# Kernel optimization log

Hardware: AMD Instinct MI355X
Metric: run time of the kernel (lower is better)

Reference implementation:

```python
import jax, jax.numpy as jnp
import numpy as np

D = 512; H = 8; DFF = 2048; S1 = 1024; S2 = 512; B = 8; EPS = 1e-5


def setup_inputs() -> dict:
    key = jax.random.key(0)
    ks = jax.random.split(key, 10)
    def w(k, shape):
        return jax.random.normal(k, shape, dtype=jnp.float32) * 0.02
    return {
        "rna_embed": jax.random.normal(ks[0], (S1, B, D), dtype=jnp.float32),
        "protein_embed": jax.random.normal(ks[1], (S2, B, D), dtype=jnp.float32),
        # self-attention params (torch MHA packed in_proj)
        "Wqkv_s": w(ks[2], (3 * D, D)), "bqkv_s": jnp.zeros((3 * D,), jnp.float32),
        "Wo_s": w(ks[3], (D, D)), "bo_s": jnp.zeros((D,), jnp.float32),
        # cross-attention params
        "Wqkv_c": w(ks[4], (3 * D, D)), "bqkv_c": jnp.zeros((3 * D,), jnp.float32),
        "Wo_c": w(ks[5], (D, D)), "bo_c": jnp.zeros((D,), jnp.float32),
        # FFN params
        "W1": w(ks[6], (DFF, D)), "b1": jnp.zeros((DFF,), jnp.float32),
        "W2": w(ks[7], (D, DFF)), "b2": jnp.zeros((D,), jnp.float32),
        # LayerNorm params: norm0_1, norm1_1, norm1_2, norm2
        "g0": jnp.ones((D,), jnp.float32), "be0": jnp.zeros((D,), jnp.float32),
        "g11": jnp.ones((D,), jnp.float32), "be11": jnp.zeros((D,), jnp.float32),
        "g12": jnp.ones((D,), jnp.float32), "be12": jnp.zeros((D,), jnp.float32),
        "g2": jnp.ones((D,), jnp.float32), "be2": jnp.zeros((D,), jnp.float32),
    }


def _layernorm(x, g, b):
    m = jnp.mean(x, axis=-1, keepdims=True)
    v = jnp.mean(jnp.square(x - m), axis=-1, keepdims=True)
    return (x - m) * jax.lax.rsqrt(v + EPS) * g + b


def _mha(xq, xkv, Wqkv, bqkv, Wo, bo):
    # xq: (Sq, B, D), xkv: (Sk, B, D)
    Wq, Wk, Wv = jnp.split(Wqkv, 3, axis=0)
    bq, bk, bv = jnp.split(bqkv, 3)
    hd = D // H
    scale = 1.0 / np.sqrt(hd).astype(np.float32)
    q = (xq @ Wq.T + bq).reshape(xq.shape[0], -1, H, hd)   # (Sq,B,H,hd)
    k = (xkv @ Wk.T + bk).reshape(xkv.shape[0], -1, H, hd)  # (Sk,B,H,hd)
    v = (xkv @ Wv.T + bv).reshape(xkv.shape[0], -1, H, hd)
    scores = jnp.einsum('qbhd,kbhd->bhqk', q, k) * scale    # (B,H,Sq,Sk)
    attn = jax.nn.softmax(scores, axis=-1)
    o = jnp.einsum('bhqk,kbhd->qbhd', attn, v).reshape(xq.shape[0], -1, D)
    return o @ Wo.T + bo


def reference(rna_embed, protein_embed, Wqkv_s, bqkv_s, Wo_s, bo_s,
              Wqkv_c, bqkv_c, Wo_c, bo_c, W1, b1, W2, b2,
              g0, be0, g11, be11, g12, be12, g2, be2):
    x1 = rna_embed
    # pre-norm self-attention
    h = _layernorm(x1, g0, be0)
    x1 = x1 + _mha(h, h, Wqkv_s, bqkv_s, Wo_s, bo_s)
    # pre-norm cross-attention (queries from x1, keys/values from protein)
    x1 = x1 + _mha(_layernorm(x1, g11, be11), _layernorm(protein_embed, g12, be12),
                   Wqkv_c, bqkv_c, Wo_c, bo_c)
    # pre-norm FFN
    h = _layernorm(x1, g2, be2)
    x1 = x1 + (jax.nn.relu(h @ W1.T + b1) @ W2.T + b2)
    return x1
```

## Files before the change

kernel.cpp:

```cpp
#include <hip/hip_runtime.h>

typedef unsigned short u16;
typedef unsigned int u32;
typedef u16 u16x8 __attribute__((ext_vector_type(8)));
typedef u16 u16x4 __attribute__((ext_vector_type(4)));
typedef short bfx8 __attribute__((ext_vector_type(8)));
typedef float f32x4 __attribute__((ext_vector_type(4)));

#define AS1 __attribute__((address_space(1)))
#define AS3 __attribute__((address_space(3)))

__device__ __forceinline__ u16 f2bf(float f) {
  union { float f; u32 u; } c; c.f = f;
  u32 u = c.u;
  u += 0x7fffu + ((u >> 16) & 1u);
  return (u16)(u >> 16);
}

__device__ __forceinline__ float bf2f(u16 b) {
  union { u32 u; float f; } c; c.u = ((u32)b) << 16;
  return c.f;
}

__device__ __forceinline__ u32 cvt_pk_bf16(float lo, float hi) {
  u32 r;
  asm("v_cvt_pk_bf16_f32 %0, %1, %2" : "=v"(r) : "v"(lo), "v"(hi));
  return r;
}

__device__ __forceinline__ float fexp2(float x) {
  float r;
  asm("v_exp_f32 %0, %1" : "=v"(r) : "v"(x));
  return r;
}

__device__ __forceinline__ void ln_core(float f[8], const float* __restrict__ g,
                                        const float* __restrict__ be,
                                        u16* __restrict__ out, int gw, int lane) {
  float s = 0.f, q = 0.f;
#pragma unroll
  for (int e = 0; e < 8; ++e) { s += f[e]; q += f[e] * f[e]; }
#pragma unroll
  for (int m = 1; m < 64; m <<= 1) { s += __shfl_xor(s, m); q += __shfl_xor(q, m); }
  float mean = s * (1.f / 512.f);
  float var = q * (1.f / 512.f) - mean * mean;
  float rs = rsqrtf(var + 1e-5f);
  const float4* g4 = (const float4*)g;
  const float4* b4 = (const float4*)be;
  float4 ga = g4[2 * lane], gb = g4[2 * lane + 1];
  float4 ba = b4[2 * lane], bb = b4[2 * lane + 1];
  float gv[8] = {ga.x, ga.y, ga.z, ga.w, gb.x, gb.y, gb.z, gb.w};
  float bv[8] = {ba.x, ba.y, ba.z, ba.w, bb.x, bb.y, bb.z, bb.w};
  u16x8 o;
#pragma unroll
  for (int e = 0; e < 8; ++e) o[e] = f2bf((f[e] - mean) * rs * gv[e] + bv[e]);
  ((u16x8*)(out + (size_t)gw * 512))[lane] = o;
}

__device__ __forceinline__ void ln_row_f32(const float* __restrict__ x, const float* __restrict__ g,
                                           const float* __restrict__ be, u16* __restrict__ out,
                                           int gw, int lane) {
  const float4* row = (const float4*)(x + (size_t)gw * 512);
  float4 a = row[2 * lane], b = row[2 * lane + 1];
  float f[8] = {a.x, a.y, a.z, a.w, b.x, b.y, b.z, b.w};
  ln_core(f, g, be, out, gw, lane);
}

__device__ __forceinline__ void ln_row_bf16(const u16* __restrict__ x, const float* __restrict__ g,
                                            const float* __restrict__ be, u16* __restrict__ out,
                                            int gw, int lane) {
  u16x8 v = ((const u16x8*)(x + (size_t)gw * 512))[lane];
  float f[8];
#pragma unroll
  for (int e = 0; e < 8; ++e) f[e] = bf2f(v[e]);
  ln_core(f, g, be, out, gw, lane);
}

__global__ __launch_bounds__(256) void cvtln_kernel(const float* __restrict__ a0, const float* __restrict__ a1,
                                                    const float* __restrict__ a2, const float* __restrict__ a3,
                                                    const float* __restrict__ a4, const float* __restrict__ a5,
                                                    u16* __restrict__ b0, u16* __restrict__ b1,
                                                    u16* __restrict__ b2, u16* __restrict__ b3,
                                                    u16* __restrict__ b4, u16* __restrict__ b5,
                                                    const float* __restrict__ x, const float* __restrict__ g,
                                                    const float* __restrict__ be, u16* __restrict__ lnout) {
  if (blockIdx.x < 4096) {
    int i = blockIdx.x * 256 + threadIdx.x;
    const float* s; u16* d; int off;
    if      (i < 196608) { s = a0; d = b0; off = i; }
    else if (i < 262144) { s = a1; d = b1; off = i - 196608; }
    else if (i < 458752) { s = a2; d = b2; off = i - 262144; }
    else if (i < 524288) { s = a3; d = b3; off = i - 458752; }
    else if (i < 786432) { s = a4; d = b4; off = i - 524288; }
    else                 { s = a5; d = b5; off = i - 786432; }
    float4 v = ((const float4*)s)[off];
    u16x4 o;
    o[0] = f2bf(v.x); o[1] = f2bf(v.y); o[2] = f2bf(v.z); o[3] = f2bf(v.w);
    ((u16x4*)d)[off] = o;
  } else {
    int gw = ((blockIdx.x - 4096) * 256 + threadIdx.x) >> 6;
    ln_row_f32(x, g, be, lnout, gw, threadIdx.x & 63);
  }
}

__global__ __launch_bounds__(256) void lnb_kernel(const u16* __restrict__ x,
                                                  const float* __restrict__ g,
                                                  const float* __restrict__ be,
                                                  u16* __restrict__ out, int ntok) {
  int gw = (blockIdx.x * 256 + threadIdx.x) >> 6;
  if (gw >= ntok) return;
  ln_row_bf16(x, g, be, out, gw, threadIdx.x & 63);
}

__global__ __launch_bounds__(256) void ln2_kernel(const u16* __restrict__ xa, const float* __restrict__ ga,
                                                  const float* __restrict__ ba, u16* __restrict__ oa,
                                                  const float* __restrict__ xb, const float* __restrict__ gb,
                                                  const float* __restrict__ bb, u16* __restrict__ ob) {
  int lane = threadIdx.x & 63;
  if (blockIdx.x < 2048) {
    int gw = (blockIdx.x * 256 + threadIdx.x) >> 6;
    ln_row_bf16(xa, ga, ba, oa, gw, lane);
  } else {
    int gw = ((blockIdx.x - 2048) * 256 + threadIdx.x) >> 6;
    ln_row_f32(xb, gb, bb, ob, gw, lane);
  }
}

__global__ __launch_bounds__(256) void vt_kernel(const u16* __restrict__ vB, u16* __restrict__ vt,
                                                 int stride, int S) {
  __shared__ u16 lt[64 * 68];
  const int t = threadIdx.x;
  const int b = blockIdx.y, h = blockIdx.z;
  const int sr = t >> 3, dc = (t & 7) * 8;
#pragma unroll
  for (int p = 0; p < 2; ++p) {
    int s = blockIdx.x * 64 + sr + p * 32;
    u16x8 v = *(const u16x8*)(vB + (size_t)(s * 8 + b) * stride + h * 64 + dc);
    u16x4 lo, hi;
    lo[0]=v[0]; lo[1]=v[1]; lo[2]=v[2]; lo[3]=v[3];
    hi[0]=v[4]; hi[1]=v[5]; hi[2]=v[6]; hi[3]=v[7];
    *(u16x4*)&lt[(sr + p * 32) * 68 + dc] = lo;
    *(u16x4*)&lt[(sr + p * 32) * 68 + dc + 4] = hi;
  }
  __syncthreads();
#pragma unroll
  for (int p = 0; p < 2; ++p) {
    int d = sr + p * 32;
    u16x8 o;
#pragma unroll
    for (int e = 0; e < 8; ++e) o[e] = lt[(dc + e) * 68 + d];
    *(u16x8*)(vt + ((size_t)(b * 8 + h) * 64 + d) * S + blockIdx.x * 64 + dc) = o;
  }
}

template <int EPI, int BM, int BN>
__device__ __forceinline__ void gemm8_body(const u16* __restrict__ A,
                                           const u16* __restrict__ Bw,
                                           const float* __restrict__ bias,
                                           const void* __restrict__ res,
                                           void* __restrict__ Cout,
                                           int M, int K, int bn, int bm) {
  constexpr int WCg = BN / 64;
  constexpr int WRg = 8 / WCg;
  constexpr int RPW = BM / WRg;
  constexpr int IM = RPW / 16;
  constexpr int LD = (BM + BN) / 64;
  __shared__ __align__(16) u16 lA[2][BM * 64];
  __shared__ __align__(16) u16 lB[2][BN * 64];
  const int tid = threadIdx.x;
  const int lane = tid & 63, w = tid >> 6;
  const int wr = w / WCg, wc = w % WCg;
  const int r15 = lane & 15, kg = lane >> 4;
  const int xr = (r15 & 7) << 4;

  f32x4 acc[IM][4] = {};

  const int lrw = tid >> 3;
  const int lcl = ((tid & 7) * 8) ^ ((lrw & 7) * 8);
  const u16* gA = A + (size_t)(bn + lrw) * K + lcl;
  const u16* gB = Bw + (size_t)(bm + lrw) * K + lcl;
  const int ldsbase = (w * 8) * 64;

#define STAGE8(buf, t) do {                                                               \
    _Pragma("unroll")                                                                     \
    for (int i_ = 0; i_ < BM / 64; ++i_)                                                  \
      __builtin_amdgcn_global_load_lds((AS1 u32*)(gA + (size_t)(i_ * 64) * K + (t) * 64), \
                                       (AS3 u32*)&lA[buf][i_ * 4096 + ldsbase], 16, 0, 0);\
    _Pragma("unroll")                                                                     \
    for (int i_ = 0; i_ < BN / 64; ++i_)                                                  \
      __builtin_amdgcn_global_load_lds((AS1 u32*)(gB + (size_t)(i_ * 64) * K + (t) * 64), \
                                       (AS3 u32*)&lB[buf][i_ * 4096 + ldsbase], 16, 0, 0);\
  } while (0)

  const int nk = K >> 6;
  STAGE8(0, 0);
  for (int t = 0; t < nk; ++t) {
    const int cur = t & 1;
    if (t + 1 < nk) {
      STAGE8(cur ^ 1, t + 1);
      if constexpr (LD == 3)      asm volatile("s_waitcnt vmcnt(3)" ::: "memory");
      else if constexpr (LD == 4) asm volatile("s_waitcnt vmcnt(4)" ::: "memory");
      else                        asm volatile("s_waitcnt vmcnt(8)" ::: "memory");
    } else {
      asm volatile("s_waitcnt vmcnt(0)" ::: "memory");
    }
    __builtin_amdgcn_sched_barrier(0);
    __builtin_amdgcn_s_barrier();
    __builtin_amdgcn_sched_barrier(0);

    const char* Ac = (const char*)lA[cur];
    const char* Bc = (const char*)lB[cur];
    __builtin_amdgcn_s_setprio(1);
#pragma unroll
    for (int kk = 0; kk < 2; ++kk) {
      bfx8 a[IM], b[4];
#pragma unroll
      for (int i = 0; i < IM; ++i)
        a[i] = *(const bfx8*)(Ac + (wr * RPW + i * 16 + r15) * 128 + ((kk * 64 + kg * 16) ^ xr));
#pragma unroll
      for (int j = 0; j < 4; ++j)
        b[j] = *(const bfx8*)(Bc + (wc * 64 + j * 16 + r15) * 128 + ((kk * 64 + kg * 16) ^ xr));
#pragma unroll
      for (int i = 0; i < IM; ++i)
#pragma unroll
        for (int j = 0; j < 4; ++j)
          acc[i][j] = __builtin_amdgcn_mfma_f32_16x16x32_bf16(a[i], b[j], acc[i][j], 0, 0, 0);
    }
    __builtin_amdgcn_s_setprio(0);
    __builtin_amdgcn_sched_barrier(0);
    __builtin_amdgcn_s_barrier();
  }
#undef STAGE8

#pragma unroll
  for (int i = 0; i < IM; ++i) {
#pragma unroll
    for (int j = 0; j < 4; ++j) {
      int col = bm + wc * 64 + j * 16 + r15;
      float bv = bias[col];
#pragma unroll
      for (int r = 0; r < 4; ++r) {
        int row = bn + wr * RPW + i * 16 + kg * 4 + r;
        size_t idx = (size_t)row * M + col;
        float v = acc[i][j][r] + bv;
        if (EPI == 1) v = fmaxf(v, 0.f);
        if (EPI == 3) {
          ((u16*)Cout)[idx] = f2bf(((const float*)res)[idx] + v);
        } else if (EPI == 4) {
          ((u16*)Cout)[idx] = f2bf(bf2f(((const u16*)res)[idx]) + v);
        } else if (EPI == 5) {
          ((float*)Cout)[idx] = bf2f(((const u16*)res)[idx]) + v;
        } else {
          ((u16*)Cout)[idx] = f2bf(v);
        }
      }
    }
  }
}

template <int EPI, int BM, int BN, int MINW>
__global__ __launch_bounds__(512, MINW) void gemm8(const u16* __restrict__ A,
                                                   const u16* __restrict__ Bw,
                                                   const float* __restrict__ bias,
                                                   const void* __restrict__ res,
                                                   void* __restrict__ Cout,
                                                   int N, int M, int K) {
  const int nwg = gridDim.x * gridDim.y;
  const int id = blockIdx.y * gridDim.x + blockIdx.x;
  const int swz = (id & 7) * (nwg >> 3) + (id >> 3);
  const int bn = (swz / gridDim.x) * BM;
  const int bm = (swz % gridDim.x) * BN;
  gemm8_body<EPI, BM, BN>(A, Bw, bias, res, Cout, M, K, bn, bm);
}

__global__ __launch_bounds__(512, 6) void gemm8_dual(const u16* __restrict__ A0, const u16* __restrict__ W0,
                                                     const float* __restrict__ c0, u16* __restrict__ O0,
                                                     const u16* __restrict__ A1, const u16* __restrict__ W1,
                                                     const float* __restrict__ c1, u16* __restrict__ O1) {
  const int id = blockIdx.x;
  const u16 *A, *Bw; const float* bias; u16* C; int M, gx, lid;
  if (id < 512) { A = A0; Bw = W0; bias = c0; C = O0; M = 512;  gx = 4; lid = id; }
  else          { A = A1; Bw = W1; bias = c1; C = O1; M = 1024; gx = 8; lid = id - 512; }
  const int swz = (lid & 7) * 64 + (lid >> 3);
  const int bn = (swz / gx) * 64;
  const int bm = (swz % gx) * 128;
  gemm8_body<0, 64, 128>(A, Bw, bias, nullptr, C, M, 512, bn, bm);
}

__global__ __launch_bounds__(512, 4) void attn_kernel(const u16* __restrict__ qB,
                                                      const u16* __restrict__ kB,
                                                      const u16* __restrict__ vtB,
                                                      u16* __restrict__ oB,
                                                      int qStride, int kvStride, int Sk) {
  __shared__ __align__(16) u16 lK[4][64 * 64];
  __shared__ __align__(16) u16 lVt[4][64 * 64];
  const int tid = threadIdx.x, lane = tid & 63, w = tid >> 6;
  const int sid = blockIdx.x;
  const int h = sid & 7, b = (sid >> 3) & 7, qt = sid >> 6;
  const int r15 = lane & 15, kg = lane >> 4;
  const int srow = lane >> 3;
  const int sxcol = ((lane & 7) * 8) ^ (srow * 8);

  const int qs = qt * 128 + w * 16 + r15;
  const u16* qrow = qB + (size_t)(qs * 8 + b) * qStride + h * 64;
  bfx8 qf0 = *(const bfx8*)(qrow + kg * 8);
  bfx8 qf1 = *(const bfx8*)(qrow + 32 + kg * 8);

  const int rl = w * 8 + srow;
  const int krow = (rl & 32) | ((rl & 12) << 1) | ((rl & 16) >> 2) | (rl & 3);

  const u16* vbase = vtB + ((size_t)(b * 8 + h) * 64) * Sk;
  const u16* kp0 = kB + ((size_t)krow * 8 + b) * kvStride + h * 64 + sxcol;
  const size_t kAdv = (size_t)64 * 8 * kvStride;
  const u16* vp0 = vbase + (size_t)rl * Sk + sxcol;

#define STAGE(buf, tt) do {                                                           \
    __builtin_amdgcn_global_load_lds((AS1 u32*)(kp0 + (size_t)(tt) * kAdv),           \
                                     (AS3 u32*)&lK[buf][(w * 8) * 64], 16, 0, 0);     \
    __builtin_amdgcn_global_load_lds((AS1 u32*)(vp0 + (size_t)(tt) * 64),             \
                                     (AS3 u32*)&lVt[buf][(w * 8) * 64], 16, 0, 0);    \
  } while (0)

  const int nt = Sk / 64;
  const int np = nt >> 1;
  STAGE(0, 0); STAGE(1, 1);

  f32x4 oacc[4] = {};
  float mrow = -1e30f, lsum = 0.f;
  const float C2 = 0.125f * 1.44269504088896340736f;
  const int xr = (r15 & 7) << 4;

  for (int i = 0; i < np; ++i) {
    const int ba = (i & 1) * 2, bb = ba + 1;
    __builtin_amdgcn_sched_barrier(0);
    __builtin_amdgcn_s_barrier();
    __builtin_amdgcn_sched_barrier(0);
    if (i + 1 < np) {
      const int sb = ((i + 1) & 1) * 2;
      STAGE(sb, 2 * (i + 1)); STAGE(sb + 1, 2 * (i + 1) + 1);
      asm volatile("s_waitcnt vmcnt(4)" ::: "memory");
    } else {
      asm volatile("s_waitcnt vmcnt(0)" ::: "memory");
    }
    __builtin_amdgcn_sched_barrier(0);

    const char* Ka = (const char*)lK[ba];
    const char* Kb = (const char*)lK[bb];
    f32x4 sa[4] = {}, sb_[4] = {};
    __builtin_amdgcn_s_setprio(1);
#pragma unroll
    for (int j = 0; j < 4; ++j) {
      const char* kpa = Ka + (j * 16 + r15) * 128;
      bfx8 ka0 = *(const bfx8*)(kpa + ((kg * 16) ^ xr));
      bfx8 ka1 = *(const bfx8*)(kpa + ((64 + kg * 16) ^ xr));
      sa[j] = __builtin_amdgcn_mfma_f32_16x16x32_bf16(ka0, qf0, sa[j], 0, 0, 0);
      sa[j] = __builtin_amdgcn_mfma_f32_16x16x32_bf16(ka1, qf1, sa[j], 0, 0, 0);
    }
#pragma unroll
    for (int j = 0; j < 4; ++j) {
      const char* kpb = Kb + (j * 16 + r15) * 128;
      bfx8 kb0 = *(const bfx8*)(kpb + ((kg * 16) ^ xr));
      bfx8 kb1 = *(const bfx8*)(kpb + ((64 + kg * 16) ^ xr));
      sb_[j] = __builtin_amdgcn_mfma_f32_16x16x32_bf16(kb0, qf0, sb_[j], 0, 0, 0);
      sb_[j] = __builtin_amdgcn_mfma_f32_16x16x32_bf16(kb1, qf1, sb_[j], 0, 0, 0);
    }
    __builtin_amdgcn_s_setprio(0);

    float lm = fmaxf(fmaxf(fmaxf(sa[0][0], sa[0][1]), fmaxf(sa[0][2], sa[0][3])),
              fmaxf(fmaxf(fmaxf(sa[1][0], sa[1][1]), fmaxf(sa[1][2], sa[1][3])),
              fmaxf(fmaxf(fmaxf(sa[2][0], sa[2][1]), fmaxf(sa[2][2], sa[2][3])),
                    fmaxf(fmaxf(sa[3][0], sa[3][1]), fmaxf(sa[3][2], sa[3][3])))));
    float lmb = fmaxf(fmaxf(fmaxf(sb_[0][0], sb_[0][1]), fmaxf(sb_[0][2], sb_[0][3])),
               fmaxf(fmaxf(fmaxf(sb_[1][0], sb_[1][1]), fmaxf(sb_[1][2], sb_[1][3])),
               fmaxf(fmaxf(fmaxf(sb_[2][0], sb_[2][1]), fmaxf(sb_[2][2], sb_[2][3])),
                     fmaxf(fmaxf(sb_[3][0], sb_[3][1]), fmaxf(sb_[3][2], sb_[3][3])))));
    lm = fmaxf(lm, lmb);

    if (!__all(lm <= mrow + 16.0f)) {
      float m0 = fmaxf(lm, __shfl_xor(lm, 16));
      m0 = fmaxf(m0, __shfl_xor(m0, 32));
      float mn = fmaxf(mrow, m0);
      float corr = fexp2((mrow - mn) * C2);
      mrow = mn;
      lsum *= corr;
#pragma unroll
      for (int jd = 0; jd < 4; ++jd)
#pragma unroll
        for (int r = 0; r < 4; ++r) oacc[jd][r] *= corr;
    }
    float bc = -mrow * C2;

    float pa[4][4], pb[4][4];
#pragma unroll
    for (int j = 0; j < 4; ++j)
#pragma unroll
      for (int r = 0; r < 4; ++r) {
        pa[j][r] = fexp2(fmaf(sa[j][r], C2, bc));
        pb[j][r] = fexp2(fmaf(sb_[j][r], C2, bc));
      }
    float ps = 0.f;
#pragma unroll
    for (int j = 0; j < 4; ++j)
#pragma unroll
      for (int r = 0; r < 4; ++r) ps += pa[j][r] + pb[j][r];
    lsum += ps;

    const char* Va = (const char*)lVt[ba];
    __builtin_amdgcn_s_setprio(1);
#pragma unroll
    for (int s2 = 0; s2 < 2; ++s2) {
      union { u32 u[4]; bfx8 v; } pt;
      pt.u[0] = cvt_pk_bf16(pa[2 * s2][0],     pa[2 * s2][1]);
      pt.u[1] = cvt_pk_bf16(pa[2 * s2][2],     pa[2 * s2][3]);
      pt.u[2] = cvt_pk_bf16(pa[2 * s2 + 1][0], pa[2 * s2 + 1][1]);
      pt.u[3] = cvt_pk_bf16(pa[2 * s2 + 1][2], pa[2 * s2 + 1][3]);
#pragma unroll
      for (int jd = 0; jd < 4; ++jd) {
        const char* vp = Va + (jd * 16 + r15) * 128;
        bfx8 vf = *(const bfx8*)(vp + ((s2 * 64 + kg * 16) ^ xr));
        oacc[jd] = __builtin_amdgcn_mfma_f32_16x16x32_bf16(vf, pt.v, oacc[jd], 0, 0, 0);
      }
    }
    __builtin_amdgcn_s_setprio(0);

    const char* Vb = (const char*)lVt[bb];
    __builtin_amdgcn_s_setprio(1);
#pragma unroll
    for (int s2 = 0; s2 < 2; ++s2) {
      union { u32 u[4]; bfx8 v; } pt;
      pt.u[0] = cvt_pk_bf16(pb[2 * s2][0],     pb[2 * s2][1]);
      pt.u[1] = cvt_pk_bf16(pb[2 * s2][2],     pb[2 * s2][3]);
      pt.u[2] = cvt_pk_bf16(pb[2 * s2 + 1][0], pb[2 * s2 + 1][1]);
      pt.u[3] = cvt_pk_bf16(pb[2 * s2 + 1][2], pb[2 * s2 + 1][3]);
#pragma unroll
      for (int jd = 0; jd < 4; ++jd) {
        const char* vp = Vb + (jd * 16 + r15) * 128;
        bfx8 vf = *(const bfx8*)(vp + ((s2 * 64 + kg * 16) ^ xr));
        oacc[jd] = __builtin_amdgcn_mfma_f32_16x16x32_bf16(vf, pt.v, oacc[jd], 0, 0, 0);
      }
    }
    __builtin_amdgcn_s_setprio(0);
  }
#undef STAGE

  lsum += __shfl_xor(lsum, 16);
  lsum += __shfl_xor(lsum, 32);
  float inv = 1.f / lsum;
  const int s = qt * 128 + w * 16 + r15;
  u16* orow = oB + (size_t)(s * 8 + b) * 512 + h * 64;
#pragma unroll
  for (int jd = 0; jd < 4; ++jd) {
    u32 p0 = cvt_pk_bf16(oacc[jd][0] * inv, oacc[jd][1] * inv);
    u32 p1 = cvt_pk_bf16(oacc[jd][2] * inv, oacc[jd][3] * inv);
    *(u32*)(orow + jd * 16 + kg * 4) = p0;
    *(u32*)(orow + jd * 16 + kg * 4 + 2) = p1;
  }
}

extern "C" void kernel_launch(void* const* d_in, const int* in_sizes, int n_in,
                              void* d_out, int out_size, void* d_ws, size_t ws_size,
                              hipStream_t stream) {
  const float* rna    = (const float*)d_in[0];
  const float* prot   = (const float*)d_in[1];
  const float* Wqkv_s = (const float*)d_in[2];
  const float* bqkv_s = (const float*)d_in[3];
  const float* Wo_s   = (const float*)d_in[4];
  const float* bo_s   = (const float*)d_in[5];
  const float* Wqkv_c = (const float*)d_in[6];
  const float* bqkv_c = (const float*)d_in[7];
  const float* Wo_c   = (const float*)d_in[8];
  const float* bo_c   = (const float*)d_in[9];
  const float* W1     = (const float*)d_in[10];
  const float* b1     = (const float*)d_in[11];
  const float* W2     = (const float*)d_in[12];
  const float* b2     = (const float*)d_in[13];
  const float* g0  = (const float*)d_in[14];
  const float* be0 = (const float*)d_in[15];
  const float* g11 = (const float*)d_in[16];
  const float* be11= (const float*)d_in[17];
  const float* g12 = (const float*)d_in[18];
  const float* be12= (const float*)d_in[19];
  const float* g2  = (const float*)d_in[20];
  const float* be2 = (const float*)d_in[21];
  float* out = (float*)d_out;

  u16* wbf      = (u16*)d_ws;
  u16* w_qkv_s  = wbf;
  u16* w_o_s    = wbf + 786432;
  u16* w_qkv_c  = wbf + 1048576;
  u16* w_o_c    = wbf + 1835008;
  u16* w_1      = wbf + 2097152;
  u16* w_2      = wbf + 3145728;
  u16* hbuf     = wbf + 4194304;
  u16* qkv      = hbuf + 4194304;
  u16* kvc      = qkv + 4194304;
  u16* attnO    = qkv + 12582912;
  u16* hp       = attnO + 4194304;
  u16* x1b      = hp + 2097152;
  u16* x1c      = x1b + 4194304;
  u16* ffnmid   = qkv;

  cvtln_kernel<<<6144, 256, 0, stream>>>(Wqkv_s, Wo_s, Wqkv_c, Wo_c, W1, W2,
                                         w_qkv_s, w_o_s, w_qkv_c, w_o_c, w_1, w_2,
                                         rna, g0, be0, hbuf);

  gemm8<0, 128, 128, 4><<<dim3(12, 64), 512, 0, stream>>>(hbuf, w_qkv_s, bqkv_s, nullptr, qkv, 8192, 1536, 512);
  vt_kernel<<<dim3(16, 8, 8), 256, 0, stream>>>(qkv + 1024, hbuf, 1536, 1024);
  attn_kernel<<<512, 512, 0, stream>>>(qkv, qkv + 512, hbuf, attnO, 1536, 1536, 1024);
  gemm8<3, 64, 128, 6><<<dim3(4, 128), 512, 0, stream>>>(attnO, w_o_s, bo_s, rna, x1b, 8192, 512, 512);

  ln2_kernel<<<3072, 256, 0, stream>>>(x1b, g11, be11, hbuf, prot, g12, be12, hp);
  gemm8_dual<<<1024, 512, 0, stream>>>(hbuf, w_qkv_c, bqkv_c, qkv,
                                       hp, w_qkv_c + 512 * 512, bqkv_c + 512, kvc);
  vt_kernel<<<dim3(8, 8, 8), 256, 0, stream>>>(kvc + 512, hp, 1024, 512);
  attn_kernel<<<512, 512, 0, stream>>>(qkv, kvc, hp, attnO, 512, 1024, 512);
  gemm8<4, 64, 128, 6><<<dim3(4, 128), 512, 0, stream>>>(attnO, w_o_c, bo_c, x1b, x1c, 8192, 512, 512);

  lnb_kernel<<<2048, 256, 0, stream>>>(x1c, g2, be2, hbuf, 8192);
  gemm8<1, 256, 256, 2><<<dim3(8, 32), 512, 0, stream>>>(hbuf, w_1, b1, nullptr, ffnmid, 8192, 2048, 512);
  gemm8<5, 64, 128, 6><<<dim3(4, 128), 512, 0, stream>>>(ffnmid, w_2, b2, x1c, out, 8192, 512, 2048);
}
```

Measured before the change: 188.0 us.

## Process two query tiles per wave in attention to reuse K/V loads

Each attention wave now handles 32 query rows instead of 16, using two independent online-softmax accumulators. Every K and V fragment read from LDS therefore feeds two MFMAs, and the grid is halved to 256 blocks with launch bounds relaxed to 2 blocks per CU. This cuts LDS traffic and global K/V staging per query, at the cost of higher register pressure, lower occupancy and fewer blocks to fill the GPU. The FFN first GEMM also moves from 256x256 to 128x128 tiles for more blocks.

After: 188.0 us. Within noise of the previous version (+0.0%).

```diff
diff --git a/kernel.cpp b/kernel.cpp
--- a/kernel.cpp
+++ b/kernel.cpp
@@ -287,7 +287,7 @@
   gemm8_body<0, 64, 128>(A, Bw, bias, nullptr, C, M, 512, bn, bm);
 }
 
-__global__ __launch_bounds__(512, 4) void attn_kernel(const u16* __restrict__ qB,
+__global__ __launch_bounds__(512, 2) void attn_kernel(const u16* __restrict__ qB,
                                                       const u16* __restrict__ kB,
                                                       const u16* __restrict__ vtB,
                                                       u16* __restrict__ oB,
@@ -301,10 +301,13 @@
   const int srow = lane >> 3;
   const int sxcol = ((lane & 7) * 8) ^ (srow * 8);
 
-  const int qs = qt * 128 + w * 16 + r15;
-  const u16* qrow = qB + (size_t)(qs * 8 + b) * qStride + h * 64;
-  bfx8 qf0 = *(const bfx8*)(qrow + kg * 8);
-  bfx8 qf1 = *(const bfx8*)(qrow + 32 + kg * 8);
+  const int q0 = qt * 256 + w * 32 + r15;
+  const u16* qrow0 = qB + (size_t)(q0 * 8 + b) * qStride + h * 64;
+  const u16* qrow1 = qB + (size_t)((q0 + 16) * 8 + b) * qStride + h * 64;
+  bfx8 qf0a = *(const bfx8*)(qrow0 + kg * 8);
+  bfx8 qf0b = *(const bfx8*)(qrow0 + 32 + kg * 8);
+  bfx8 qf1a = *(const bfx8*)(qrow1 + kg * 8);
+  bfx8 qf1b = *(const bfx8*)(qrow1 + 32 + kg * 8);
 
   const int rl = w * 8 + srow;
   const int krow = (rl & 32) | ((rl & 12) << 1) | ((rl & 16) >> 2) | (rl & 3);
@@ -325,13 +328,12 @@
   const int np = nt >> 1;
   STAGE(0, 0); STAGE(1, 1);
 
-  f32x4 oacc[4] = {};
-  float mrow = -1e30f, lsum = 0.f;
+  f32x4 oacc0[4] = {}, oacc1[4] = {};
+  float mrow0 = -1e30f, mrow1 = -1e30f, lsum0 = 0.f, lsum1 = 0.f;
   const float C2 = 0.125f * 1.44269504088896340736f;
   const int xr = (r15 & 7) << 4;
 
   for (int i = 0; i < np; ++i) {
-    const int ba = (i & 1) * 2, bb = ba + 1;
     __builtin_amdgcn_sched_barrier(0);
     __builtin_amdgcn_s_barrier();
     __builtin_amdgcn_sched_barrier(0);
@@ -344,116 +346,110 @@
     }
     __builtin_amdgcn_sched_barrier(0);
 
-    const char* Ka = (const char*)lK[ba];
-    const char* Kb = (const char*)lK[bb];
-    f32x4 sa[4] = {}, sb_[4] = {};
-    __builtin_amdgcn_s_setprio(1);
-#pragma unroll
-    for (int j = 0; j < 4; ++j) {
-      const char* kpa = Ka + (j * 16 + r15) * 128;
-      bfx8 ka0 = *(const bfx8*)(kpa + ((kg * 16) ^ xr));
-      bfx8 ka1 = *(const bfx8*)(kpa + ((64 + kg * 16) ^ xr));
-      sa[j] = __builtin_amdgcn_mfma_f32_16x16x32_bf16(ka0, qf0, sa[j], 0, 0, 0);
-      sa[j] = __builtin_amdgcn_mfma_f32_16x16x32_bf16(ka1, qf1, sa[j], 0, 0, 0);
+#pragma unroll
+    for (int tb = 0; tb < 2; ++tb) {
+      const int buf = (i & 1) * 2 + tb;
+      const char* Kc = (const char*)lK[buf];
+      const char* Vc = (const char*)lVt[buf];
+
+      f32x4 s0[4] = {}, s1[4] = {};
+      __builtin_amdgcn_s_setprio(1);
+#pragma unroll
+      for (int j = 0; j < 4; ++j) {
+        const char* kp = Kc + (j * 16 + r15) * 128;
+        bfx8 kf0 = *(const bfx8*)(kp + ((kg * 16) ^ xr));
+        bfx8 kf1 = *(const bfx8*)(kp + ((64 + kg * 16) ^ xr));
+        s0[j] = __builtin_amdgcn_mfma_f32_16x16x32_bf16(kf0, qf0a, s0[j], 0, 0, 0);
+        s0[j] = __builtin_amdgcn_mfma_f32_16x16x32_bf16(kf1, qf0b, s0[j], 0, 0, 0);
+        s1[j] = __builtin_amdgcn_mfma_f32_16x16x32_bf16(kf0, qf1a, s1[j], 0, 0, 0);
+        s1[j] = __builtin_amdgcn_mfma_f32_16x16x32_bf16(kf1, qf1b, s1[j], 0, 0, 0);
+      }
+      __builtin_amdgcn_s_setprio(0);
+
+      float lm0 = fmaxf(fmaxf(fmaxf(s0[0][0], s0[0][1]), fmaxf(s0[0][2], s0[0][3])),
+                 fmaxf(fmaxf(fmaxf(s0[1][0], s0[1][1]), fmaxf(s0[1][2], s0[1][3])),
+                 fmaxf(fmaxf(fmaxf(s0[2][0], s0[2][1]), fmaxf(s0[2][2], s0[2][3])),
+                       fmaxf(fmaxf(s0[3][0], s0[3][1]), fmaxf(s0[3][2], s0[3][3])))));
+      if (!__all(lm0 <= mrow0 + 16.0f)) {
+        float m0 = fmaxf(lm0, __shfl_xor(lm0, 16));
+        m0 = fmaxf(m0, __shfl_xor(m0, 32));
+        float mn = fmaxf(mrow0, m0);
+        float corr = fexp2((mrow0 - mn) * C2);
+        mrow0 = mn;
+        lsum0 *= corr;
+#pragma unroll
+        for (int jd = 0; jd < 4; ++jd)
+#pragma unroll
+          for (int r = 0; r < 4; ++r) oacc0[jd][r] *= corr;
+      }
+      float lm1 = fmaxf(fmaxf(fmaxf(s1[0][0], s1[0][1]), fmaxf(s1[0][2], s1[0][3])),
+                 fmaxf(fmaxf(fmaxf(s1[1][0], s1[1][1]), fmaxf(s1[1][2], s1[1][3])),
+                 fmaxf(fmaxf(fmaxf(s1[2][0], s1[2][1]), fmaxf(s1[2][2], s1[2][3])),
+                       fmaxf(fmaxf(s1[3][0], s1[3][1]), fmaxf(s1[3][2], s1[3][3])))));
+      if (!__all(lm1 <= mrow1 + 16.0f)) {
+        float m1 = fmaxf(lm1, __shfl_xor(lm1, 16));
+        m1 = fmaxf(m1, __shfl_xor(m1, 32));
+        float mn = fmaxf(mrow1, m1);
+        float corr = fexp2((mrow1 - mn) * C2);
+        mrow1 = mn;
+        lsum1 *= corr;
+#pragma unroll
+        for (int jd = 0; jd < 4; ++jd)
+#pragma unroll
+          for (int r = 0; r < 4; ++r) oacc1[jd][r] *= corr;
+      }
+
+      float bc0 = -mrow0 * C2, bc1 = -mrow1 * C2;
+      float p0[4][4], p1[4][4];
+      float ps0 = 0.f, ps1 = 0.f;
+#pragma unroll
+      for (int j = 0; j < 4; ++j)
+#pragma unroll
+        for (int r = 0; r < 4; ++r) {
+          p0[j][r] = fexp2(fmaf(s0[j][r], C2, bc0));
+          p1[j][r] = fexp2(fmaf(s1[j][r], C2, bc1));
+          ps0 += p0[j][r]; ps1 += p1[j][r];
+        }
+      lsum0 += ps0; lsum1 += ps1;
+
+      __builtin_amdgcn_s_setprio(1);
+#pragma unroll
+      for (int s2 = 0; s2 < 2; ++s2) {
+        union { u32 u[4]; bfx8 v; } pt0, pt1;
+        pt0.u[0] = cvt_pk_bf16(p0[2 * s2][0],     p0[2 * s2][1]);
+        pt0.u[1] = cvt_pk_bf16(p0[2 * s2][2],     p0[2 * s2][3]);
+        pt0.u[2] = cvt_pk_bf16(p0[2 * s2 + 1][0], p0[2 * s2 + 1][1]);
+        pt0.u[3] = cvt_pk_bf16(p0[2 * s2 + 1][2], p0[2 * s2 + 1][3]);
+        pt1.u[0] = cvt_pk_bf16(p1[2 * s2][0],     p1[2 * s2][1]);
+        pt1.u[1] = cvt_pk_bf16(p1[2 * s2][2],     p1[2 * s2][3]);
+        pt1.u[2] = cvt_pk_bf16(p1[2 * s2 + 1][0], p1[2 * s2 + 1][1]);
+        pt1.u[3] = cvt_pk_bf16(p1[2 * s2 + 1][2], p1[2 * s2 + 1][3]);
+#pragma unroll
+        for (int jd = 0; jd < 4; ++jd) {
+          const char* vp = Vc + (jd * 16 + r15) * 128;
+          bfx8 vf = *(const bfx8*)(vp + ((s2 * 64 + kg * 16) ^ xr));
+          oacc0[jd] = __builtin_amdgcn_mfma_f32_16x16x32_bf16(vf, pt0.v, oacc0[jd], 0, 0, 0);
+          oacc1[jd] = __builtin_amdgcn_mfma_f32_16x16x32_bf16(vf, pt1.v, oacc1[jd], 0, 0, 0);
+        }
+      }
+      __builtin_amdgcn_s_setprio(0);
     }
-#pragma unroll
-    for (int j = 0; j < 4; ++j) {
-      const char* kpb = Kb + (j * 16 + r15) * 128;
-      bfx8 kb0 = *(const bfx8*)(kpb + ((kg * 16) ^ xr));
-      bfx8 kb1 = *(const bfx8*)(kpb + ((64 + kg * 16) ^ xr));
-      sb_[j] = __builtin_amdgcn_mfma_f32_16x16x32_bf16(kb0, qf0, sb_[j], 0, 0, 0);
-      sb_[j] = __builtin_amdgcn_mfma_f32_16x16x32_bf16(kb1, qf1, sb_[j], 0, 0, 0);
-    }
-    __builtin_amdgcn_s_setprio(0);
-
-    float lm = fmaxf(fmaxf(fmaxf(sa[0][0], sa[0][1]), fmaxf(sa[0][2], sa[0][3])),
-              fmaxf(fmaxf(fmaxf(sa[1][0], sa[1][1]), fmaxf(sa[1][2], sa[1][3])),
-              fmaxf(fmaxf(fmaxf(sa[2][0], sa[2][1]), fmaxf(sa[2][2], sa[2][3])),
-                    fmaxf(fmaxf(sa[3][0], sa[3][1]), fmaxf(sa[3][2], sa[3][3])))));
-    float lmb = fmaxf(fmaxf(fmaxf(sb_[0][0], sb_[0][1]), fmaxf(sb_[0][2], sb_[0][3])),
-               fmaxf(fmaxf(fmaxf(sb_[1][0], sb_[1][1]), fmaxf(sb_[1][2], sb_[1][3])),
-               fmaxf(fmaxf(fmaxf(sb_[2][0], sb_[2][1]), fmaxf(sb_[2][2], sb_[2][3])),
-                     fmaxf(fmaxf(sb_[3][0], sb_[3][1]), fmaxf(sb_[3][2], sb_[3][3])))));
-    lm = fmaxf(lm, lmb);
-
-    if (!__all(lm <= mrow + 16.0f)) {
-      float m0 = fmaxf(lm, __shfl_xor(lm, 16));
-      m0 = fmaxf(m0, __shfl_xor(m0, 32));
-      float mn = fmaxf(mrow, m0);
-      float corr = fexp2((mrow - mn) * C2);
-      mrow = mn;
-      lsum *= corr;
-#pragma unroll
-      for (int jd = 0; jd < 4; ++jd)
-#pragma unroll
-        for (int r = 0; r < 4; ++r) oacc[jd][r] *= corr;
-    }
-    float bc = -mrow * C2;
-
-    float pa[4][4], pb[4][4];
-#pragma unroll
-    for (int j = 0; j < 4; ++j)
-#pragma unroll
-      for (int r = 0; r < 4; ++r) {
-        pa[j][r] = fexp2(fmaf(sa[j][r], C2, bc));
-        pb[j][r] = fexp2(fmaf(sb_[j][r], C2, bc));
-      }
-    float ps = 0.f;
-#pragma unroll
-    for (int j = 0; j < 4; ++j)
-#pragma unroll
-      for (int r = 0; r < 4; ++r) ps += pa[j][r] + pb[j][r];
-    lsum += ps;
-
-    const char* Va = (const char*)lVt[ba];
-    __builtin_amdgcn_s_setprio(1);
-#pragma unroll
-    for (int s2 = 0; s2 < 2; ++s2) {
-      union { u32 u[4]; bfx8 v; } pt;
-      pt.u[0] = cvt_pk_bf16(pa[2 * s2][0],     pa[2 * s2][1]);
-      pt.u[1] = cvt_pk_bf16(pa[2 * s2][2],     pa[2 * s2][3]);
-      pt.u[2] = cvt_pk_bf16(pa[2 * s2 + 1][0], pa[2 * s2 + 1][1]);
-      pt.u[3] = cvt_pk_bf16(pa[2 * s2 + 1][2], pa[2 * s2 + 1][3]);
-#pragma unroll
-      for (int jd = 0; jd < 4; ++jd) {
-        const char* vp = Va + (jd * 16 + r15) * 128;
-        bfx8 vf = *(const bfx8*)(vp + ((s2 * 64 + kg * 16) ^ xr));
-        oacc[jd] = __builtin_amdgcn_mfma_f32_16x16x32_bf16(vf, pt.v, oacc[jd], 0, 0, 0);
-      }
-    }
-    __builtin_amdgcn_s_setprio(0);
-
-    const char* Vb = (const char*)lVt[bb];
-    __builtin_amdgcn_s_setprio(1);
-#pragma unroll
-    for (int s2 = 0; s2 < 2; ++s2) {
-      union { u32 u[4]; bfx8 v; } pt;
-      pt.u[0] = cvt_pk_bf16(pb[2 * s2][0],     pb[2 * s2][1]);
-      pt.u[1] = cvt_pk_bf16(pb[2 * s2][2],     pb[2 * s2][3]);
-      pt.u[2] = cvt_pk_bf16(pb[2 * s2 + 1][0], pb[2 * s2 + 1][1]);
-      pt.u[3] = cvt_pk_bf16(pb[2 * s2 + 1][2], pb[2 * s2 + 1][3]);
-#pragma unroll
-      for (int jd = 0; jd < 4; ++jd) {
-        const char* vp = Vb + (jd * 16 + r15) * 128;
-        bfx8 vf = *(const bfx8*)(vp + ((s2 * 64 + kg * 16) ^ xr));
-        oacc[jd] = __builtin_amdgcn_mfma_f32_16x16x32_bf16(vf, pt.v, oacc[jd], 0, 0, 0);
-      }
-    }
-    __builtin_amdgcn_s_setprio(0);
   }
 #undef STAGE
 
-  lsum += __shfl_xor(lsum, 16);
-  lsum += __shfl_xor(lsum, 32);
-  float inv = 1.f / lsum;
-  const int s = qt * 128 + w * 16 + r15;
-  u16* orow = oB + (size_t)(s * 8 + b) * 512 + h * 64;
+  lsum0 += __shfl_xor(lsum0, 16);
+  lsum0 += __shfl_xor(lsum0, 32);
+  lsum1 += __shfl_xor(lsum1, 16);
+  lsum1 += __shfl_xor(lsum1, 32);
+  float inv0 = 1.f / lsum0, inv1 = 1.f / lsum1;
+  u16* orow0 = oB + (size_t)(q0 * 8 + b) * 512 + h * 64;
+  u16* orow1 = oB + (size_t)((q0 + 16) * 8 + b) * 512 + h * 64;
 #pragma unroll
   for (int jd = 0; jd < 4; ++jd) {
-    u32 p0 = cvt_pk_bf16(oacc[jd][0] * inv, oacc[jd][1] * inv);
-    u32 p1 = cvt_pk_bf16(oacc[jd][2] * inv, oacc[jd][3] * inv);
-    *(u32*)(orow + jd * 16 + kg * 4) = p0;
-    *(u32*)(orow + jd * 16 + kg * 4 + 2) = p1;
+    *(u32*)(orow0 + jd * 16 + kg * 4)     = cvt_pk_bf16(oacc0[jd][0] * inv0, oacc0[jd][1] * inv0);
+    *(u32*)(orow0 + jd * 16 + kg * 4 + 2) = cvt_pk_bf16(oacc0[jd][2] * inv0, oacc0[jd][3] * inv0);
+    *(u32*)(orow1 + jd * 16 + kg * 4)     = cvt_pk_bf16(oacc1[jd][0] * inv1, oacc1[jd][1] * inv1);
+    *(u32*)(orow1 + jd * 16 + kg * 4 + 2) = cvt_pk_bf16(oacc1[jd][2] * inv1, oacc1[jd][3] * inv1);
   }
 }
 
@@ -506,17 +502,17 @@
 
   gemm8<0, 128, 128, 4><<<dim3(12, 64), 512, 0, stream>>>(hbuf, w_qkv_s, bqkv_s, nullptr, qkv, 8192, 1536, 512);
   vt_kernel<<<dim3(16, 8, 8), 256, 0, stream>>>(qkv + 1024, hbuf, 1536, 1024);
-  attn_kernel<<<512, 512, 0, stream>>>(qkv, qkv + 512, hbuf, attnO, 1536, 1536, 1024);
+  attn_kernel<<<256, 512, 0, stream>>>(qkv, qkv + 512, hbuf, attnO, 1536, 1536, 1024);
   gemm8<3, 64, 128, 6><<<dim3(4, 128), 512, 0, stream>>>(attnO, w_o_s, bo_s, rna, x1b, 8192, 512, 512);
 
   ln2_kernel<<<3072, 256, 0, stream>>>(x1b, g11, be11, hbuf, prot, g12, be12, hp);
   gemm8_dual<<<1024, 512, 0, stream>>>(hbuf, w_qkv_c, bqkv_c, qkv,
                                        hp, w_qkv_c + 512 * 512, bqkv_c + 512, kvc);
   vt_kernel<<<dim3(8, 8, 8), 256, 0, stream>>>(kvc + 512, hp, 1024, 512);
-  attn_kernel<<<512, 512, 0, stream>>>(qkv, kvc, hp, attnO, 512, 1024, 512);
+  attn_kernel<<<256, 512, 0, stream>>>(qkv, kvc, hp, attnO, 512, 1024, 512);
   gemm8<4, 64, 128, 6><<<dim3(4, 128), 512, 0, stream>>>(attnO, w_o_c, bo_c, x1b, x1c, 8192, 512, 512);
 
   lnb_kernel<<<2048, 256, 0, stream>>>(x1c, g2, be2, hbuf, 8192);
-  gemm8<1, 256, 256, 2><<<dim3(8, 32), 512, 0, stream>>>(hbuf, w_1, b1, nullptr, ffnmid, 8192, 2048, 512);
+  gemm8<1, 128, 128, 4><<<dim3(16, 64), 512, 0, stream>>>(hbuf, w_1, b1, nullptr, ffnmid, 8192, 2048, 512);
   gemm8<5, 64, 128, 6><<<dim3(4, 128), 512, 0, stream>>>(ffnmid, w_2, b2, x1c, out, 8192, 512, 2048);
 }
```
